# Kernel optimization log

Hardware: AMD Instinct MI355X
Metric: run time of the kernel (lower is better)

## Reference

```python
import jax, jax.numpy as jnp
import numpy as np
import math

B = 2048
STEP = 2        # candidate restarts (original hardcodes 100)
DDIM = 20       # DDIM reverse steps
TIME_DIM = 512
STATE = 6
ACT = 8


def _ddim_coeffs():
    # noise schedule from sample_backward (numpy, host-side constants)
    T = 1000
    t = np.arange(1, T + 1, dtype=np.float64)
    b_max, b_min = 10.0, 0.1
    alpha = np.exp(-b_min / T - 0.5 * (b_max - b_min) * (2 * t - 1) / T ** 2)
    ap = np.cumprod(alpha)
    ts = np.linspace(T, 0, DDIM + 1).astype(np.int64)
    coeffs = []
    for i in range(1, DDIM + 1):
        cur = int(ts[i - 1] - 1)
        prev = int(ts[i] - 1)
        ab_c = ap[cur]
        ab_p = ap[prev] if prev >= 0 else 1.0
        c1 = (ab_p / ab_c) ** 0.5
        var = (1 - ab_p) / (1 - ab_c) * (1 - ab_c / ab_p)  # eta=1 (simple_var)
        c2 = max(1 - ab_p - var, 0.0) ** 0.5 - (ab_p * (1 - ab_c) / ab_c) ** 0.5
        c3 = (1 - ab_c / ab_p) ** 0.5                      # simple_var third term
        coeffs.append((float(cur), float(c1), float(c2), float(c3)))
    return coeffs

_COEFFS = _ddim_coeffs()

_PI = math.pi
JOINT_HIGH = np.array([35 * _PI / 180, -60 * _PI / 180, 3.94, 155 * _PI / 180,
                       -55 * _PI / 180, _PI, 5 * _PI / 180, 3.71], dtype=np.float32)
JOINT_LOW = np.array([-35 * _PI / 180, -155 * _PI / 180, 2.59, 60 * _PI / 180,
                      -125 * _PI / 180, -_PI, -90 * _PI / 180, 2.50], dtype=np.float32)


def _time_emb(cur_t):
    # sinusoidal encoding of a scalar timestep, interleaved sin/cos -> [TIME_DIM]
    div = jnp.exp(jnp.arange(0, TIME_DIM, 2, dtype=jnp.float32) * (-math.log(10000.0) / TIME_DIM))
    return jnp.stack([jnp.sin(cur_t * div), jnp.cos(cur_t * div)], axis=1).reshape(-1)


def _fk(joints):
    # DH forward kinematics over 8 joints; joints: [B, 8] -> pose [B, 6]
    q1, q2, d3, q4, q5, q6, q7, d8 = (joints[:, k] for k in range(8))
    zeros = jnp.zeros_like(q1)
    ones = jnp.ones_like(q1)
    alpha = jnp.deg2rad(jnp.array([0., -90., -90., 90., -90., -90., 90., -90.], dtype=jnp.float32))
    a = jnp.array([0., 0.16, 0.07, 0., 0.1334, 0., 0.15, 0.3625], dtype=jnp.float32)
    d = jnp.stack([zeros, zeros, d3, zeros, -0.1316 * ones, 1.0105 * ones, 0.52 * ones, d8], axis=1)  # [B,8]
    th = jnp.stack([q1, q2, zeros, q4, q5, q6, q7, zeros], axis=1)  # [B,8]
    ct, st = jnp.cos(th), jnp.sin(th)
    ca, sa = jnp.cos(alpha), jnp.sin(alpha)  # [8]
    z8 = jnp.zeros_like(ct)
    o8 = jnp.ones_like(ct)
    ab = jnp.broadcast_to(a, ct.shape)
    row0 = jnp.stack([ct, -st, z8, ab], axis=-1)
    row1 = jnp.stack([st * ca, ct * ca, -sa * o8, -sa * d], axis=-1)
    row2 = jnp.stack([st * sa, ct * sa, ca * o8, ca * d], axis=-1)
    row3 = jnp.stack([z8, z8, z8, o8], axis=-1)
    M = jnp.stack([row0, row1, row2, row3], axis=2)  # [B, 8, 4, 4]
    T = M[:, 0]
    for j in range(1, 8):  # fixed tiny chain of 7 bmms
        T = T @ M[:, j]
    R = T[:, :3, :3]
    hole = jnp.array([0., 0., 3.75], dtype=jnp.float32)
    e1 = R @ hole  # [B, 3]
    pose = jnp.stack([T[:, 0, 3], T[:, 1, 3], T[:, 2, 3] + 1.702,
                      e1[:, 0] + T[:, 0, 3], e1[:, 1] + T[:, 1, 3], e1[:, 2] + T[:, 2, 3] + 1.702], axis=1)
    return pose


def setup_inputs() -> dict:
    key = jax.random.key(0)
    ks = jax.random.split(key, 16)

    def w(k, i, o):
        return jax.random.normal(k, (i, o), jnp.float32) / float(np.sqrt(i))

    return {
        "x_pre": jax.random.normal(ks[0], (B, STATE), jnp.float32) * 50.0,
        "noise": jax.random.normal(ks[1], (STEP, B, ACT), jnp.float32),
        "W_in": w(ks[2], STATE + ACT + TIME_DIM, 512), "b_in": jnp.zeros((512,), jnp.float32),
        "W1": w(ks[3], 512, 512), "b1": jnp.zeros((512,), jnp.float32),
        "W2": w(ks[4], 512, 512), "b2": jnp.zeros((512,), jnp.float32),
        "W3": w(ks[5], 512, 512), "b3": jnp.zeros((512,), jnp.float32),
        "W4": w(ks[6], 512, 512), "b4": jnp.zeros((512,), jnp.float32),
        "W_out": w(ks[7], 512, ACT), "b_out": jnp.zeros((ACT,), jnp.float32),
    }


def reference(x_pre, noise, W_in, b_in, W1, b1, W2, b2, W3, b3, W4, b4, W_out, b_out):
    gelu = lambda v: jax.nn.gelu(v, approximate=False)

    def denoiser(state, action, cur_t):
        t_emb = jnp.broadcast_to(_time_emb(cur_t), (state.shape[0], TIME_DIM))
        x = jnp.concatenate([state, action, t_emb], axis=1)
        y = gelu(x @ W_in + b_in)
        y = gelu(y @ W1 + b1)
        y = gelu(y @ W2 + b2)
        y = gelu(y @ W3 + b3)
        y = gelu(y @ W4 + b4)
        return y @ W_out + b_out

    high = jnp.asarray(JOINT_HIGH)
    low = jnp.asarray(JOINT_LOW)

    errors, joints_all = [], []
    for s in range(STEP):
        nz = noise[s]
        # DDIM reverse loop; NB: the original never feeds z back into `noise`,
        # so each iteration denoises the same initial noise (replicated faithfully).
        z = nz
        for (cur_t, c1, c2, c3) in _COEFFS:
            joint_0 = denoiser(x_pre, nz, cur_t)
            z = c1 * nz + c2 * joint_0 + c3 * nz
        joint_normal = (jnp.tanh(z / 10.0) + 1.0) / 2.0
        new_joint = joint_normal * (high - low) + low  # [B, 8]
        pose_V = _fk(new_joint)                         # [B, 6]
        moni = 100.0 * pose_V
        dist0 = jnp.sqrt(jnp.sum((moni[:, :3] - x_pre[:, :3]) ** 2, axis=1))
        dist1 = jnp.sqrt(jnp.sum((moni[:, 3:] - x_pre[:, 3:]) ** 2, axis=1))
        errors.append(dist0 + dist1)
        joints_all.append(new_joint)

    errors = jnp.stack(errors, axis=0)        # [STEP, B]
    joints_all = jnp.stack(joints_all, axis=0)  # [STEP, B, 8]
    idx = jnp.argmin(errors, axis=0)          # per-sample best restart
    best = jnp.take_along_axis(joints_all, idx[None, :, None], axis=0)[0]  # [B, 8]
    return best
```

## Files before the change

### kernel.cpp

```cpp
#include <hip/hip_runtime.h>
#include <math.h>

typedef __bf16 bf16x8 __attribute__((ext_vector_type(8)));
typedef float f32x4 __attribute__((ext_vector_type(4)));
typedef unsigned short u16;
typedef unsigned short u16x8 __attribute__((ext_vector_type(8)));
typedef unsigned int u32;

constexpr int BATCH = 2048;
constexpr int ROWS  = 4096;
constexpr int HID   = 512;
constexpr int NACT  = 8;

__device__ __forceinline__ float gelu_f(float x) {
    return 0.5f * x * (1.0f + erff(x * 0.70710678118654752f));
}
__device__ __forceinline__ u16 f2bf(float f) {
    u32 u = __float_as_uint(f);
    return (u16)((u + 0x7FFFu + ((u >> 16) & 1u)) >> 16);
}
__device__ __forceinline__ float bf2f(u16 h) {
    return __uint_as_float(((u32)h) << 16);
}

__device__ __forceinline__ size_t fragoff(int r, int k) {
    return (size_t)(((r >> 4) * 16 + (k >> 5)) * 512
                    + (((k & 31) >> 3) * 16 + (r & 15)) * 8 + (k & 7));
}

__global__ __launch_bounds__(256) void k_prep(
        const float* __restrict__ W1, const float* __restrict__ W2,
        const float* __restrict__ W3, const float* __restrict__ W4,
        const float* __restrict__ W_in,
        u16* __restrict__ wt, float* __restrict__ partials) {
    int z = blockIdx.z;
    if (z == 4) {
        if (blockIdx.x >= 4 || blockIdx.y != 0) return;
        __shared__ float temb[128];
        int x = blockIdx.x, t = threadIdx.x;
        if (t < 128) {
            int k = x * 128 + t;
            int p = k >> 1;
            float div = expf((float)(2 * p) * (-9.210340371976184f / 512.0f));
            temb[t] = (k & 1) ? cosf(49.0f * div) : sinf(49.0f * div);
        }
        __syncthreads();
#pragma unroll
        for (int half = 0; half < 2; ++half) {
            int col = half * 256 + t;
            float acc = 0.f;
            for (int kk = 0; kk < 128; ++kk)
                acc += temb[kk] * W_in[(size_t)(14 + x * 128 + kk) * HID + col];
            partials[x * HID + col] = acc;
        }
        return;
    }
    __shared__ float tile[32][33];
    const float* Ws[4] = {W1, W2, W3, W4};
    const float* W = Ws[z];
    u16* wh = wt + (size_t)z * 524288;
    u16* wl = wh + 262144;
    int kt = blockIdx.x * 32, nt = blockIdx.y * 32, t = threadIdx.x;
    int c = t & 31, r = t >> 5;
#pragma unroll
    for (int p = 0; p < 4; ++p)
        tile[r + p * 8][c] = W[(size_t)(kt + r + p * 8) * HID + nt + c];
    __syncthreads();
#pragma unroll
    for (int p = 0; p < 4; ++p) {
        int nl = r + p * 8, kl = c;
        float v = tile[kl][nl];
        u16 h = f2bf(v);
        u16 l2 = f2bf(v - bf2f(h));
        size_t o = fragoff(nt + nl, kt + kl);
        wh[o] = h;
        wl[o] = l2;
    }
}

__global__ __launch_bounds__(256) void k_layer_in(
        const float* __restrict__ x_pre, const float* __restrict__ noise,
        const float* __restrict__ W_in, const float* __restrict__ b_in,
        const float* __restrict__ partials,
        u16* __restrict__ Yh, u16* __restrict__ Yl) {
    int id = blockIdx.x * 256 + threadIdx.x;
    int r = id >> 6, oct = id & 63;
    int s = r >> 11, bidx = r & 2047;
    float xv[6], nz[8];
#pragma unroll
    for (int j = 0; j < 6; ++j) xv[j] = x_pre[bidx * 6 + j];
#pragma unroll
    for (int j = 0; j < 8; ++j) nz[j] = noise[(s * BATCH + bidx) * NACT + j];
    int nc = oct * 8;
    float acc[8];
#pragma unroll
    for (int q = 0; q < 2; ++q) {
        float4 bv = *(const float4*)&b_in[nc + q * 4];
        float4 p0 = *(const float4*)&partials[nc + q * 4];
        float4 p1 = *(const float4*)&partials[512 + nc + q * 4];
        float4 p2 = *(const float4*)&partials[1024 + nc + q * 4];
        float4 p3 = *(const float4*)&partials[1536 + nc + q * 4];
        acc[q * 4 + 0] = bv.x + p0.x + p1.x + p2.x + p3.x;
        acc[q * 4 + 1] = bv.y + p0.y + p1.y + p2.y + p3.y;
        acc[q * 4 + 2] = bv.z + p0.z + p1.z + p2.z + p3.z;
        acc[q * 4 + 3] = bv.w + p0.w + p1.w + p2.w + p3.w;
    }
#pragma unroll
    for (int j = 0; j < 14; ++j) {
        float xj = (j < 6) ? xv[j] : nz[j - 6];
        float4 wa = *(const float4*)&W_in[j * HID + nc];
        float4 wb = *(const float4*)&W_in[j * HID + nc + 4];
        acc[0] += xj * wa.x; acc[1] += xj * wa.y;
        acc[2] += xj * wa.z; acc[3] += xj * wa.w;
        acc[4] += xj * wb.x; acc[5] += xj * wb.y;
        acc[6] += xj * wb.z; acc[7] += xj * wb.w;
    }
    u16x8 hv, lv;
#pragma unroll
    for (int j2 = 0; j2 < 8; ++j2) {
        float g = gelu_f(acc[j2]);
        u16 hi = f2bf(g);
        hv[j2] = hi;
        lv[j2] = f2bf(g - bf2f(hi));
    }
    size_t o = fragoff(r, nc);
    *(u16x8*)&Yh[o] = hv;
    *(u16x8*)&Yl[o] = lv;
}

__global__ __launch_bounds__(512) void k_gemm_f(
        const u16* __restrict__ Ah, const u16* __restrict__ Al,
        const u16* __restrict__ Wh, const u16* __restrict__ Wl,
        const float* __restrict__ bias,
        u16* __restrict__ Yh, u16* __restrict__ Yl) {
    __shared__ __align__(16) u16 lds[3][4][4][512];
    int tid = threadIdx.x, lane = tid & 63, w = tid >> 6;
    int wm = w >> 1, wn = w & 1;
    int m0 = blockIdx.x * 64, n0 = blockIdx.y * 64;

    int p  = w >> 1;
    int g0 = (w & 1) * 2;
    const u16* pl = (p == 0) ? Ah : (p == 1) ? Al : (p == 2) ? Wh : Wl;
    int grpb = ((p < 2) ? m0 : n0) >> 4;
    const u16* src0 = pl + (size_t)((grpb + g0) * 16) * 512 + lane * 8;
    const u16* src1 = pl + (size_t)((grpb + g0 + 1) * 16) * 512 + lane * 8;

    auto stage = [&](int c, int bb) {
        __builtin_amdgcn_global_load_lds(
            (const __attribute__((address_space(1))) void*)(src0 + c * 512),
            (__attribute__((address_space(3))) void*)&lds[bb][p][g0][0], 16, 0, 0);
        __builtin_amdgcn_global_load_lds(
            (const __attribute__((address_space(1))) void*)(src1 + c * 512),
            (__attribute__((address_space(3))) void*)&lds[bb][p][g0 + 1][0], 16, 0, 0);
    };

    f32x4 zero = {0.f, 0.f, 0.f, 0.f};
    f32x4 acc[2] = {zero, zero};

    stage(0, 0);
    stage(1, 1);
#pragma unroll
    for (int c = 0; c < 16; ++c) {
        int bb = c % 3;
        if (c < 15) { asm volatile("s_waitcnt vmcnt(2)" ::: "memory"); }
        else        { asm volatile("s_waitcnt vmcnt(0)" ::: "memory"); }
        __builtin_amdgcn_s_barrier();
        __builtin_amdgcn_sched_barrier(0);

        bf16x8 ah = *(const bf16x8*)&lds[bb][0][wm][lane * 8];
        bf16x8 al = *(const bf16x8*)&lds[bb][1][wm][lane * 8];
        bf16x8 bh[2], bl[2];
#pragma unroll
        for (int j = 0; j < 2; ++j) {
            bh[j] = *(const bf16x8*)&lds[bb][2][wn * 2 + j][lane * 8];
            bl[j] = *(const bf16x8*)&lds[bb][3][wn * 2 + j][lane * 8];
        }
        __builtin_amdgcn_s_setprio(1);
#pragma unroll
        for (int j = 0; j < 2; ++j) {
            acc[j] = __builtin_amdgcn_mfma_f32_16x16x32_bf16(ah, bh[j], acc[j], 0, 0, 0);
            acc[j] = __builtin_amdgcn_mfma_f32_16x16x32_bf16(ah, bl[j], acc[j], 0, 0, 0);
            acc[j] = __builtin_amdgcn_mfma_f32_16x16x32_bf16(al, bh[j], acc[j], 0, 0, 0);
        }
        __builtin_amdgcn_s_setprio(0);
        __builtin_amdgcn_sched_barrier(0);
        if (c < 14) stage(c + 2, (c + 2) % 3);
    }

    int row0 = m0 + wm * 16 + (lane >> 4) * 4;
#pragma unroll
    for (int j = 0; j < 2; ++j) {
        int col = n0 + wn * 32 + j * 16 + (lane & 15);
        float bia = bias[col];
#pragma unroll
        for (int r2 = 0; r2 < 4; ++r2) {
            float g = gelu_f(acc[j][r2] + bia);
            u16 hi = f2bf(g);
            size_t o = fragoff(row0 + r2, col);
            Yh[o] = hi;
            Yl[o] = f2bf(g - bf2f(hi));
        }
    }
}

__device__ void mat4mul(float C[4][4], const float A[4][4], const float Bm[4][4]) {
#pragma unroll
    for (int i = 0; i < 4; ++i)
#pragma unroll
        for (int j = 0; j < 4; ++j) {
            float s = A[i][0] * Bm[0][j];
            s += A[i][1] * Bm[1][j];
            s += A[i][2] * Bm[2][j];
            s += A[i][3] * Bm[3][j];
            C[i][j] = s;
        }
}

__global__ __launch_bounds__(256) void k_out_fk(
        const u16* __restrict__ Yh, const u16* __restrict__ Yl,
        const float* __restrict__ W_out, const float* __restrict__ b_out,
        const float* __restrict__ noise, const float* __restrict__ x_pre,
        float* __restrict__ out, float c1, float c2, float c3) {
    int b = blockIdx.x * 4 + (threadIdx.x >> 6);
    int lane = threadIdx.x & 63;

    float acc0[8] = {0, 0, 0, 0, 0, 0, 0, 0};
    float acc1[8] = {0, 0, 0, 0, 0, 0, 0, 0};
#pragma unroll
    for (int it = 0; it < 8; ++it) {
        int k = lane + it * 64;
        size_t o0 = fragoff(b, k);
        size_t o1 = fragoff(BATCH + b, k);
        float ya = bf2f(Yh[o0]) + bf2f(Yl[o0]);
        float yb = bf2f(Yh[o1]) + bf2f(Yl[o1]);
        float4 w0 = ((const float4*)&W_out[k * NACT])[0];
        float4 w1 = ((const float4*)&W_out[k * NACT])[1];
        acc0[0] += ya * w0.x; acc0[1] += ya * w0.y; acc0[2] += ya * w0.z; acc0[3] += ya * w0.w;
        acc0[4] += ya * w1.x; acc0[5] += ya * w1.y; acc0[6] += ya * w1.z; acc0[7] += ya * w1.w;
        acc1[0] += yb * w0.x; acc1[1] += yb * w0.y; acc1[2] += yb * w0.z; acc1[3] += yb * w0.w;
        acc1[4] += yb * w1.x; acc1[5] += yb * w1.y; acc1[6] += yb * w1.z; acc1[7] += yb * w1.w;
    }
#pragma unroll
    for (int n = 0; n < 8; ++n) {
#pragma unroll
        for (int off = 32; off > 0; off >>= 1) {
            acc0[n] += __shfl_xor(acc0[n], off, 64);
            acc1[n] += __shfl_xor(acc1[n], off, 64);
        }
    }

    float jq[8] = {0, 0, 0, 0, 0, 0, 0, 0};
    float err = 0.f;
    if (lane < 2) {
        int s = lane;
        const float* accp = (s == 0) ? acc0 : acc1;
        const float HIf[8] = {
            (float)(35.0 * M_PI / 180.0), (float)(-60.0 * M_PI / 180.0), 3.94f,
            (float)(155.0 * M_PI / 180.0), (float)(-55.0 * M_PI / 180.0),
            (float)M_PI, (float)(5.0 * M_PI / 180.0), 3.71f};
        const float LOf[8] = {
            (float)(-35.0 * M_PI / 180.0), (float)(-155.0 * M_PI / 180.0), 2.59f,
            (float)(60.0 * M_PI / 180.0), (float)(-125.0 * M_PI / 180.0),
            (float)(-M_PI), (float)(-90.0 * M_PI / 180.0), 2.5f};
        const float* nzp = &noise[(s * BATCH + b) * NACT];
#pragma unroll
        for (int n = 0; n < 8; ++n) {
            float o = accp[n] + b_out[n];
            float z = c1 * nzp[n] + c2 * o + c3 * nzp[n];
            float jn = (tanhf(z * 0.1f) + 1.0f) * 0.5f;
            jq[n] = jn * (HIf[n] - LOf[n]) + LOf[n];
        }
        const float a_[8]  = {0.0f, 0.16f, 0.07f, 0.0f, 0.1334f, 0.0f, 0.15f, 0.3625f};
        const float ca_[8] = {1.f, 0.f, 0.f, 0.f, 0.f, 0.f, 0.f, 0.f};
        const float sa_[8] = {0.f, -1.f, -1.f, 1.f, -1.f, -1.f, 1.f, -1.f};
        float d_[8] = {0.0f, 0.0f, jq[2], 0.0f, -0.1316f, 1.0105f, 0.52f, jq[7]};
        float th[8] = {jq[0], jq[1], 0.0f, jq[3], jq[4], jq[5], jq[6], 0.0f};
        float T[4][4], M[4][4], Tn[4][4];
#pragma unroll
        for (int j = 0; j < 8; ++j) {
            float ct = cosf(th[j]);
            float st = sinf(th[j]);
            M[0][0] = ct;          M[0][1] = -st;         M[0][2] = 0.0f;    M[0][3] = a_[j];
            M[1][0] = st * ca_[j]; M[1][1] = ct * ca_[j]; M[1][2] = -sa_[j]; M[1][3] = -sa_[j] * d_[j];
            M[2][0] = st * sa_[j]; M[2][1] = ct * sa_[j]; M[2][2] = ca_[j];  M[2][3] = ca_[j] * d_[j];
            M[3][0] = 0.0f;        M[3][1] = 0.0f;        M[3][2] = 0.0f;    M[3][3] = 1.0f;
            if (j == 0) {
#pragma unroll
                for (int i = 0; i < 4; ++i)
#pragma unroll
                    for (int cc = 0; cc < 4; ++cc) T[i][cc] = M[i][cc];
            } else {
                mat4mul(Tn, T, M);
#pragma unroll
                for (int i = 0; i < 4; ++i)
#pragma unroll
                    for (int cc = 0; cc < 4; ++cc) T[i][cc] = Tn[i][cc];
            }
        }
        float e1x = T[0][2] * 3.75f;
        float e1y = T[1][2] * 3.75f;
        float e1z = T[2][2] * 3.75f;
        float p0 = T[0][3];
        float p1 = T[1][3];
        float p2 = T[2][3] + 1.702f;
        float p3 = e1x + T[0][3];
        float p4 = e1y + T[1][3];
        float p5 = e1z + T[2][3] + 1.702f;
        const float* xp = &x_pre[b * 6];
        float dx0 = 100.0f * p0 - xp[0];
        float dx1 = 100.0f * p1 - xp[1];
        float dx2 = 100.0f * p2 - xp[2];
        float dx3 = 100.0f * p3 - xp[3];
        float dx4 = 100.0f * p4 - xp[4];
        float dx5 = 100.0f * p5 - xp[5];
        err = sqrtf(dx0 * dx0 + dx1 * dx1 + dx2 * dx2) +
              sqrtf(dx3 * dx3 + dx4 * dx4 + dx5 * dx5);
    }
    float e0 = __shfl(err, 0, 64);
    float e1 = __shfl(err, 1, 64);
    int sel = (e1 < e0) ? 1 : 0;
    float jsel[8];
#pragma unroll
    for (int n = 0; n < 8; ++n) jsel[n] = __shfl(jq[n], sel, 64);
    if (lane == 0) {
#pragma unroll
        for (int n = 0; n < 8; ++n) out[b * NACT + n] = jsel[n];
    }
}

extern "C" void kernel_launch(void* const* d_in, const int* in_sizes, int n_in,
                              void* d_out, int out_size, void* d_ws, size_t ws_size,
                              hipStream_t stream) {
    const float* x_pre = (const float*)d_in[0];
    const float* noise = (const float*)d_in[1];
    const float* W_in  = (const float*)d_in[2];
    const float* b_in  = (const float*)d_in[3];
    const float* W1    = (const float*)d_in[4];
    const float* b1    = (const float*)d_in[5];
    const float* W2    = (const float*)d_in[6];
    const float* b2    = (const float*)d_in[7];
    const float* W3    = (const float*)d_in[8];
    const float* b3    = (const float*)d_in[9];
    const float* W4    = (const float*)d_in[10];
    const float* b4    = (const float*)d_in[11];
    const float* W_out = (const float*)d_in[12];
    const float* b_out = (const float*)d_in[13];

    double ab_c = exp(-0.1 * 50.0 / 1000.0 - 0.5 * (10.0 - 0.1) * 2500.0 / 1.0e6);
    float c1 = (float)sqrt(1.0 / ab_c);
    float c2 = (float)(-sqrt((1.0 - ab_c) / ab_c));
    float c3 = (float)sqrt(1.0 - ab_c);

    char* base = (char*)d_ws;
    u16* Ah = (u16*)base;
    u16* Al = Ah + 2097152;
    u16* Bh = Al + 2097152;
    u16* Bl = Bh + 2097152;
    u16* wt = (u16*)(base + 16777216);
    float* partials = (float*)(base + 16777216 + 4194304);

    k_prep<<<dim3(16, 16, 5), 256, 0, stream>>>(W1, W2, W3, W4, W_in, wt, partials);
    k_layer_in<<<ROWS * 64 / 256, 256, 0, stream>>>(x_pre, noise, W_in, b_in,
                                                    partials, Ah, Al);
    dim3 g(ROWS / 64, HID / 64);
    k_gemm_f<<<g, 512, 0, stream>>>(Ah, Al, wt + 0 * 524288, wt + 0 * 524288 + 262144, b1, Bh, Bl);
    k_gemm_f<<<g, 512, 0, stream>>>(Bh, Bl, wt + 1 * 524288, wt + 1 * 524288 + 262144, b2, Ah, Al);
    k_gemm_f<<<g, 512, 0, stream>>>(Ah, Al, wt + 2 * 524288, wt + 2 * 524288 + 262144, b3, Bh, Bl);
    k_gemm_f<<<g, 512, 0, stream>>>(Bh, Bl, wt + 3 * 524288, wt + 3 * 524288 + 262144, b4, Ah, Al);
    k_out_fk<<<BATCH / 4, 256, 0, stream>>>(Ah, Al, W_out, b_out, noise, x_pre,
                                            (float*)d_out, c1, c2, c3);
}
```

Baseline: 87.56 us.

## Retile split-bf16 GEMM to 32x128 blocks with 4 waves each owning 2x2 MFMA tiles

The hidden-layer GEMM kernel moves from 64x64 tiles with 8 waves (each computing 1x2 MFMA tiles) to 32x128 tiles with 4 waves (each computing 2x2 MFMA tiles). Each wave now reuses its A fragments across more B columns, which raises MFMA work per LDS read, and each wave issues five async global-to-LDS loads per stage instead of two. The grid grows to 128x4 blocks of 256 threads. The risk is fewer waves per block to hide latency, plus more B-weight traffic per block because each block covers a wider N range.

```diff
diff --git a/kernel.cpp b/kernel.cpp
--- a/kernel.cpp
+++ b/kernel.cpp
@@ -128,77 +128,94 @@
     *(u16x8*)&Yl[o] = lv;
 }
 
-__global__ __launch_bounds__(512) void k_gemm_f(
+__global__ __launch_bounds__(256) void k_gemm_f(
         const u16* __restrict__ Ah, const u16* __restrict__ Al,
         const u16* __restrict__ Wh, const u16* __restrict__ Wl,
         const float* __restrict__ bias,
         u16* __restrict__ Yh, u16* __restrict__ Yl) {
-    __shared__ __align__(16) u16 lds[3][4][4][512];
+    __shared__ __align__(16) u16 lds[3][20][512];
     int tid = threadIdx.x, lane = tid & 63, w = tid >> 6;
-    int wm = w >> 1, wn = w & 1;
-    int m0 = blockIdx.x * 64, n0 = blockIdx.y * 64;
-
-    int p  = w >> 1;
-    int g0 = (w & 1) * 2;
-    const u16* pl = (p == 0) ? Ah : (p == 1) ? Al : (p == 2) ? Wh : Wl;
-    int grpb = ((p < 2) ? m0 : n0) >> 4;
-    const u16* src0 = pl + (size_t)((grpb + g0) * 16) * 512 + lane * 8;
-    const u16* src1 = pl + (size_t)((grpb + g0 + 1) * 16) * 512 + lane * 8;
-
-    auto stage = [&](int c, int bb) {
-        __builtin_amdgcn_global_load_lds(
-            (const __attribute__((address_space(1))) void*)(src0 + c * 512),
-            (__attribute__((address_space(3))) void*)&lds[bb][p][g0][0], 16, 0, 0);
-        __builtin_amdgcn_global_load_lds(
-            (const __attribute__((address_space(1))) void*)(src1 + c * 512),
-            (__attribute__((address_space(3))) void*)&lds[bb][p][g0 + 1][0], 16, 0, 0);
+    int m0 = blockIdx.x * 32, n0 = blockIdx.y * 128;
+
+    int apl = w >> 1, ag = w & 1;
+    const u16* aplane = apl ? Al : Ah;
+    const u16* srcA = aplane + (size_t)((blockIdx.x * 2 + ag) * 16) * 512 + lane * 8;
+    const u16* srcB0 = Wh + (size_t)((blockIdx.y * 8 + 2 * w) * 16) * 512 + lane * 8;
+    const u16* srcB1 = Wh + (size_t)((blockIdx.y * 8 + 2 * w + 1) * 16) * 512 + lane * 8;
+    const u16* srcB2 = Wl + (size_t)((blockIdx.y * 8 + 2 * w) * 16) * 512 + lane * 8;
+    const u16* srcB3 = Wl + (size_t)((blockIdx.y * 8 + 2 * w + 1) * 16) * 512 + lane * 8;
+
+    auto stage = [&](int c, int sl) {
+        __builtin_amdgcn_global_load_lds(
+            (const __attribute__((address_space(1))) void*)(srcA + c * 512),
+            (__attribute__((address_space(3))) void*)&lds[sl][apl * 2 + ag][0], 16, 0, 0);
+        __builtin_amdgcn_global_load_lds(
+            (const __attribute__((address_space(1))) void*)(srcB0 + c * 512),
+            (__attribute__((address_space(3))) void*)&lds[sl][4 + 2 * w][0], 16, 0, 0);
+        __builtin_amdgcn_global_load_lds(
+            (const __attribute__((address_space(1))) void*)(srcB1 + c * 512),
+            (__attribute__((address_space(3))) void*)&lds[sl][4 + 2 * w + 1][0], 16, 0, 0);
+        __builtin_amdgcn_global_load_lds(
+            (const __attribute__((address_space(1))) void*)(srcB2 + c * 512),
+            (__attribute__((address_space(3))) void*)&lds[sl][12 + 2 * w][0], 16, 0, 0);
+        __builtin_amdgcn_global_load_lds(
+            (const __attribute__((address_space(1))) void*)(srcB3 + c * 512),
+            (__attribute__((address_space(3))) void*)&lds[sl][12 + 2 * w + 1][0], 16, 0, 0);
     };
 
     f32x4 zero = {0.f, 0.f, 0.f, 0.f};
-    f32x4 acc[2] = {zero, zero};
+    f32x4 acc[2][2] = {{zero, zero}, {zero, zero}};
 
     stage(0, 0);
     stage(1, 1);
 #pragma unroll
     for (int c = 0; c < 16; ++c) {
-        int bb = c % 3;
-        if (c < 15) { asm volatile("s_waitcnt vmcnt(2)" ::: "memory"); }
+        int sl = c % 3;
+        if (c < 15) { asm volatile("s_waitcnt vmcnt(5)" ::: "memory"); }
         else        { asm volatile("s_waitcnt vmcnt(0)" ::: "memory"); }
         __builtin_amdgcn_s_barrier();
         __builtin_amdgcn_sched_barrier(0);
 
-        bf16x8 ah = *(const bf16x8*)&lds[bb][0][wm][lane * 8];
-        bf16x8 al = *(const bf16x8*)&lds[bb][1][wm][lane * 8];
-        bf16x8 bh[2], bl[2];
+        bf16x8 ah[2], al[2], bh[2], bl[2];
+#pragma unroll
+        for (int i = 0; i < 2; ++i) {
+            ah[i] = *(const bf16x8*)&lds[sl][i][lane * 8];
+            al[i] = *(const bf16x8*)&lds[sl][2 + i][lane * 8];
+        }
 #pragma unroll
         for (int j = 0; j < 2; ++j) {
-            bh[j] = *(const bf16x8*)&lds[bb][2][wn * 2 + j][lane * 8];
-            bl[j] = *(const bf16x8*)&lds[bb][3][wn * 2 + j][lane * 8];
+            bh[j] = *(const bf16x8*)&lds[sl][4 + 2 * w + j][lane * 8];
+            bl[j] = *(const bf16x8*)&lds[sl][12 + 2 * w + j][lane * 8];
         }
         __builtin_amdgcn_s_setprio(1);
 #pragma unroll
-        for (int j = 0; j < 2; ++j) {
-            acc[j] = __builtin_amdgcn_mfma_f32_16x16x32_bf16(ah, bh[j], acc[j], 0, 0, 0);
-            acc[j] = __builtin_amdgcn_mfma_f32_16x16x32_bf16(ah, bl[j], acc[j], 0, 0, 0);
-            acc[j] = __builtin_amdgcn_mfma_f32_16x16x32_bf16(al, bh[j], acc[j], 0, 0, 0);
-        }
+        for (int i = 0; i < 2; ++i)
+#pragma unroll
+            for (int j = 0; j < 2; ++j) {
+                acc[i][j] = __builtin_amdgcn_mfma_f32_16x16x32_bf16(ah[i], bh[j], acc[i][j], 0, 0, 0);
+                acc[i][j] = __builtin_amdgcn_mfma_f32_16x16x32_bf16(ah[i], bl[j], acc[i][j], 0, 0, 0);
+                acc[i][j] = __builtin_amdgcn_mfma_f32_16x16x32_bf16(al[i], bh[j], acc[i][j], 0, 0, 0);
+            }
         __builtin_amdgcn_s_setprio(0);
         __builtin_amdgcn_sched_barrier(0);
         if (c < 14) stage(c + 2, (c + 2) % 3);
     }
 
-    int row0 = m0 + wm * 16 + (lane >> 4) * 4;
-#pragma unroll
-    for (int j = 0; j < 2; ++j) {
-        int col = n0 + wn * 32 + j * 16 + (lane & 15);
-        float bia = bias[col];
-#pragma unroll
-        for (int r2 = 0; r2 < 4; ++r2) {
-            float g = gelu_f(acc[j][r2] + bia);
-            u16 hi = f2bf(g);
-            size_t o = fragoff(row0 + r2, col);
-            Yh[o] = hi;
-            Yl[o] = f2bf(g - bf2f(hi));
+#pragma unroll
+    for (int i = 0; i < 2; ++i) {
+        int row0 = m0 + i * 16 + (lane >> 4) * 4;
+#pragma unroll
+        for (int j = 0; j < 2; ++j) {
+            int col = n0 + w * 32 + j * 16 + (lane & 15);
+            float bia = bias[col];
+#pragma unroll
+            for (int r2 = 0; r2 < 4; ++r2) {
+                float g = gelu_f(acc[i][j][r2] + bia);
+                u16 hi = f2bf(g);
+                size_t o = fragoff(row0 + r2, col);
+                Yh[o] = hi;
+                Yl[o] = f2bf(g - bf2f(hi));
+            }
         }
     }
 }
@@ -362,11 +379,11 @@
     k_prep<<<dim3(16, 16, 5), 256, 0, stream>>>(W1, W2, W3, W4, W_in, wt, partials);
     k_layer_in<<<ROWS * 64 / 256, 256, 0, stream>>>(x_pre, noise, W_in, b_in,
                                                     partials, Ah, Al);
-    dim3 g(ROWS / 64, HID / 64);
-    k_gemm_f<<<g, 512, 0, stream>>>(Ah, Al, wt + 0 * 524288, wt + 0 * 524288 + 262144, b1, Bh, Bl);
-    k_gemm_f<<<g, 512, 0, stream>>>(Bh, Bl, wt + 1 * 524288, wt + 1 * 524288 + 262144, b2, Ah, Al);
-    k_gemm_f<<<g, 512, 0, stream>>>(Ah, Al, wt + 2 * 524288, wt + 2 * 524288 + 262144, b3, Bh, Bl);
-    k_gemm_f<<<g, 512, 0, stream>>>(Bh, Bl, wt + 3 * 524288, wt + 3 * 524288 + 262144, b4, Ah, Al);
+    dim3 g(ROWS / 32, HID / 128);
+    k_gemm_f<<<g, 256, 0, stream>>>(Ah, Al, wt + 0 * 524288, wt + 0 * 524288 + 262144, b1, Bh, Bl);
+    k_gemm_f<<<g, 256, 0, stream>>>(Bh, Bl, wt + 1 * 524288, wt + 1 * 524288 + 262144, b2, Ah, Al);
+    k_gemm_f<<<g, 256, 0, stream>>>(Ah, Al, wt + 2 * 524288, wt + 2 * 524288 + 262144, b3, Bh, Bl);
+    k_gemm_f<<<g, 256, 0, stream>>>(Bh, Bl, wt + 3 * 524288, wt + 3 * 524288 + 262144, b4, Ah, Al);
     k_out_fk<<<BATCH / 4, 256, 0, stream>>>(Ah, Al, W_out, b_out, noise, x_pre,
                                             (float*)d_out, c1, c2, c3);
 }
```

New measurement: 93.89 us. 7.2% more time.

## Fuse input layer, four hidden GEMMs and output/FK into one persistent-row kernel

Applied to the files above, without the earlier changes.

Replaces the input-layer kernel, four tiled GEMM launches and the output/FK kernel with a single kernel where each block owns 16 rows (8 batch items × 2 restarts) and keeps the activations in LDS across all layers. Weights are streamed directly from global memory into registers with a 3-deep software prefetch, and each wave computes 64 output columns. This removes the global round-trips of the 4096×512 split-bf16 activations and five launch overheads. In exchange only 256 blocks run, every block re-reads the full weight set (served from L2), and MFMA work per block is serialized over layers with less parallelism.

```diff
diff --git a/kernel.cpp b/kernel.cpp
--- a/kernel.cpp
+++ b/kernel.cpp
@@ -8,7 +8,6 @@
 typedef unsigned int u32;
 
 constexpr int BATCH = 2048;
-constexpr int ROWS  = 4096;
 constexpr int HID   = 512;
 constexpr int NACT  = 8;
 
@@ -78,131 +77,6 @@
     }
 }
 
-__global__ __launch_bounds__(256) void k_layer_in(
-        const float* __restrict__ x_pre, const float* __restrict__ noise,
-        const float* __restrict__ W_in, const float* __restrict__ b_in,
-        const float* __restrict__ partials,
-        u16* __restrict__ Yh, u16* __restrict__ Yl) {
-    int id = blockIdx.x * 256 + threadIdx.x;
-    int r = id >> 6, oct = id & 63;
-    int s = r >> 11, bidx = r & 2047;
-    float xv[6], nz[8];
-#pragma unroll
-    for (int j = 0; j < 6; ++j) xv[j] = x_pre[bidx * 6 + j];
-#pragma unroll
-    for (int j = 0; j < 8; ++j) nz[j] = noise[(s * BATCH + bidx) * NACT + j];
-    int nc = oct * 8;
-    float acc[8];
-#pragma unroll
-    for (int q = 0; q < 2; ++q) {
-        float4 bv = *(const float4*)&b_in[nc + q * 4];
-        float4 p0 = *(const float4*)&partials[nc + q * 4];
-        float4 p1 = *(const float4*)&partials[512 + nc + q * 4];
-        float4 p2 = *(const float4*)&partials[1024 + nc + q * 4];
-        float4 p3 = *(const float4*)&partials[1536 + nc + q * 4];
-        acc[q * 4 + 0] = bv.x + p0.x + p1.x + p2.x + p3.x;
-        acc[q * 4 + 1] = bv.y + p0.y + p1.y + p2.y + p3.y;
-        acc[q * 4 + 2] = bv.z + p0.z + p1.z + p2.z + p3.z;
-        acc[q * 4 + 3] = bv.w + p0.w + p1.w + p2.w + p3.w;
-    }
-#pragma unroll
-    for (int j = 0; j < 14; ++j) {
-        float xj = (j < 6) ? xv[j] : nz[j - 6];
-        float4 wa = *(const float4*)&W_in[j * HID + nc];
-        float4 wb = *(const float4*)&W_in[j * HID + nc + 4];
-        acc[0] += xj * wa.x; acc[1] += xj * wa.y;
-        acc[2] += xj * wa.z; acc[3] += xj * wa.w;
-        acc[4] += xj * wb.x; acc[5] += xj * wb.y;
-        acc[6] += xj * wb.z; acc[7] += xj * wb.w;
-    }
-    u16x8 hv, lv;
-#pragma unroll
-    for (int j2 = 0; j2 < 8; ++j2) {
-        float g = gelu_f(acc[j2]);
-        u16 hi = f2bf(g);
-        hv[j2] = hi;
-        lv[j2] = f2bf(g - bf2f(hi));
-    }
-    size_t o = fragoff(r, nc);
-    *(u16x8*)&Yh[o] = hv;
-    *(u16x8*)&Yl[o] = lv;
-}
-
-__global__ __launch_bounds__(512) void k_gemm_f(
-        const u16* __restrict__ Ah, const u16* __restrict__ Al,
-        const u16* __restrict__ Wh, const u16* __restrict__ Wl,
-        const float* __restrict__ bias,
-        u16* __restrict__ Yh, u16* __restrict__ Yl) {
-    __shared__ __align__(16) u16 lds[3][4][4][512];
-    int tid = threadIdx.x, lane = tid & 63, w = tid >> 6;
-    int wm = w >> 1, wn = w & 1;
-    int m0 = blockIdx.x * 64, n0 = blockIdx.y * 64;
-
-    int p  = w >> 1;
-    int g0 = (w & 1) * 2;
-    const u16* pl = (p == 0) ? Ah : (p == 1) ? Al : (p == 2) ? Wh : Wl;
-    int grpb = ((p < 2) ? m0 : n0) >> 4;
-    const u16* src0 = pl + (size_t)((grpb + g0) * 16) * 512 + lane * 8;
-    const u16* src1 = pl + (size_t)((grpb + g0 + 1) * 16) * 512 + lane * 8;
-
-    auto stage = [&](int c, int bb) {
-        __builtin_amdgcn_global_load_lds(
-            (const __attribute__((address_space(1))) void*)(src0 + c * 512),
-            (__attribute__((address_space(3))) void*)&lds[bb][p][g0][0], 16, 0, 0);
-        __builtin_amdgcn_global_load_lds(
-            (const __attribute__((address_space(1))) void*)(src1 + c * 512),
-            (__attribute__((address_space(3))) void*)&lds[bb][p][g0 + 1][0], 16, 0, 0);
-    };
-
-    f32x4 zero = {0.f, 0.f, 0.f, 0.f};
-    f32x4 acc[2] = {zero, zero};
-
-    stage(0, 0);
-    stage(1, 1);
-#pragma unroll
-    for (int c = 0; c < 16; ++c) {
-        int bb = c % 3;
-        if (c < 15) { asm volatile("s_waitcnt vmcnt(2)" ::: "memory"); }
-        else        { asm volatile("s_waitcnt vmcnt(0)" ::: "memory"); }
-        __builtin_amdgcn_s_barrier();
-        __builtin_amdgcn_sched_barrier(0);
-
-        bf16x8 ah = *(const bf16x8*)&lds[bb][0][wm][lane * 8];
-        bf16x8 al = *(const bf16x8*)&lds[bb][1][wm][lane * 8];
-        bf16x8 bh[2], bl[2];
-#pragma unroll
-        for (int j = 0; j < 2; ++j) {
-            bh[j] = *(const bf16x8*)&lds[bb][2][wn * 2 + j][lane * 8];
-            bl[j] = *(const bf16x8*)&lds[bb][3][wn * 2 + j][lane * 8];
-        }
-        __builtin_amdgcn_s_setprio(1);
-#pragma unroll
-        for (int j = 0; j < 2; ++j) {
-            acc[j] = __builtin_amdgcn_mfma_f32_16x16x32_bf16(ah, bh[j], acc[j], 0, 0, 0);
-            acc[j] = __builtin_amdgcn_mfma_f32_16x16x32_bf16(ah, bl[j], acc[j], 0, 0, 0);
-            acc[j] = __builtin_amdgcn_mfma_f32_16x16x32_bf16(al, bh[j], acc[j], 0, 0, 0);
-        }
-        __builtin_amdgcn_s_setprio(0);
-        __builtin_amdgcn_sched_barrier(0);
-        if (c < 14) stage(c + 2, (c + 2) % 3);
-    }
-
-    int row0 = m0 + wm * 16 + (lane >> 4) * 4;
-#pragma unroll
-    for (int j = 0; j < 2; ++j) {
-        int col = n0 + wn * 32 + j * 16 + (lane & 15);
-        float bia = bias[col];
-#pragma unroll
-        for (int r2 = 0; r2 < 4; ++r2) {
-            float g = gelu_f(acc[j][r2] + bia);
-            u16 hi = f2bf(g);
-            size_t o = fragoff(row0 + r2, col);
-            Yh[o] = hi;
-            Yl[o] = f2bf(g - bf2f(hi));
-        }
-    }
-}
-
 __device__ void mat4mul(float C[4][4], const float A[4][4], const float Bm[4][4]) {
 #pragma unroll
     for (int i = 0; i < 4; ++i)
@@ -216,115 +90,231 @@
         }
 }
 
-__global__ __launch_bounds__(256) void k_out_fk(
-        const u16* __restrict__ Yh, const u16* __restrict__ Yl,
+__global__ __launch_bounds__(512) void k_mlp(
+        const float* __restrict__ x_pre, const float* __restrict__ noise,
+        const float* __restrict__ W_in, const float* __restrict__ b_in,
+        const float* __restrict__ partials, const u16* __restrict__ wt,
+        const float* __restrict__ b1, const float* __restrict__ b2,
+        const float* __restrict__ b3, const float* __restrict__ b4,
         const float* __restrict__ W_out, const float* __restrict__ b_out,
-        const float* __restrict__ noise, const float* __restrict__ x_pre,
         float* __restrict__ out, float c1, float c2, float c3) {
-    int b = blockIdx.x * 4 + (threadIdx.x >> 6);
-    int lane = threadIdx.x & 63;
-
-    float acc0[8] = {0, 0, 0, 0, 0, 0, 0, 0};
-    float acc1[8] = {0, 0, 0, 0, 0, 0, 0, 0};
-#pragma unroll
-    for (int it = 0; it < 8; ++it) {
-        int k = lane + it * 64;
-        size_t o0 = fragoff(b, k);
-        size_t o1 = fragoff(BATCH + b, k);
-        float ya = bf2f(Yh[o0]) + bf2f(Yl[o0]);
-        float yb = bf2f(Yh[o1]) + bf2f(Yl[o1]);
-        float4 w0 = ((const float4*)&W_out[k * NACT])[0];
-        float4 w1 = ((const float4*)&W_out[k * NACT])[1];
-        acc0[0] += ya * w0.x; acc0[1] += ya * w0.y; acc0[2] += ya * w0.z; acc0[3] += ya * w0.w;
-        acc0[4] += ya * w1.x; acc0[5] += ya * w1.y; acc0[6] += ya * w1.z; acc0[7] += ya * w1.w;
-        acc1[0] += yb * w0.x; acc1[1] += yb * w0.y; acc1[2] += yb * w0.z; acc1[3] += yb * w0.w;
-        acc1[4] += yb * w1.x; acc1[5] += yb * w1.y; acc1[6] += yb * w1.z; acc1[7] += yb * w1.w;
-    }
-#pragma unroll
-    for (int n = 0; n < 8; ++n) {
-#pragma unroll
-        for (int off = 32; off > 0; off >>= 1) {
-            acc0[n] += __shfl_xor(acc0[n], off, 64);
-            acc1[n] += __shfl_xor(acc1[n], off, 64);
-        }
-    }
-
-    float jq[8] = {0, 0, 0, 0, 0, 0, 0, 0};
-    float err = 0.f;
-    if (lane < 2) {
-        int s = lane;
-        const float* accp = (s == 0) ? acc0 : acc1;
-        const float HIf[8] = {
-            (float)(35.0 * M_PI / 180.0), (float)(-60.0 * M_PI / 180.0), 3.94f,
-            (float)(155.0 * M_PI / 180.0), (float)(-55.0 * M_PI / 180.0),
-            (float)M_PI, (float)(5.0 * M_PI / 180.0), 3.71f};
-        const float LOf[8] = {
-            (float)(-35.0 * M_PI / 180.0), (float)(-155.0 * M_PI / 180.0), 2.59f,
-            (float)(60.0 * M_PI / 180.0), (float)(-125.0 * M_PI / 180.0),
-            (float)(-M_PI), (float)(-90.0 * M_PI / 180.0), 2.5f};
-        const float* nzp = &noise[(s * BATCH + b) * NACT];
+    __shared__ __align__(16) u16 A[2][16][512];
+    int tid = threadIdx.x, lane = tid & 63, w = tid >> 6;
+    int l15 = lane & 15;
+    int b0 = blockIdx.x * 8;
+
+#pragma unroll
+    for (int rep = 0; rep < 2; ++rep) {
+        int id = tid + rep * 512;
+        int r = id & 15, oct = id >> 4;
+        int st = r >> 3, be = b0 + (r & 7);
+        float xv[6], nz[8];
+#pragma unroll
+        for (int j = 0; j < 6; ++j) xv[j] = x_pre[be * 6 + j];
+#pragma unroll
+        for (int j = 0; j < 8; ++j) nz[j] = noise[(st * BATCH + be) * NACT + j];
+        int nc = oct * 8;
+        float acc[8];
+#pragma unroll
+        for (int q = 0; q < 2; ++q) {
+            float4 bv = *(const float4*)&b_in[nc + q * 4];
+            float4 p0 = *(const float4*)&partials[nc + q * 4];
+            float4 p1 = *(const float4*)&partials[512 + nc + q * 4];
+            float4 p2 = *(const float4*)&partials[1024 + nc + q * 4];
+            float4 p3 = *(const float4*)&partials[1536 + nc + q * 4];
+            acc[q * 4 + 0] = bv.x + p0.x + p1.x + p2.x + p3.x;
+            acc[q * 4 + 1] = bv.y + p0.y + p1.y + p2.y + p3.y;
+            acc[q * 4 + 2] = bv.z + p0.z + p1.z + p2.z + p3.z;
+            acc[q * 4 + 3] = bv.w + p0.w + p1.w + p2.w + p3.w;
+        }
+#pragma unroll
+        for (int j = 0; j < 14; ++j) {
+            float xj = (j < 6) ? xv[j] : nz[j - 6];
+            float4 wa = *(const float4*)&W_in[j * HID + nc];
+            float4 wb = *(const float4*)&W_in[j * HID + nc + 4];
+            acc[0] += xj * wa.x; acc[1] += xj * wa.y;
+            acc[2] += xj * wa.z; acc[3] += xj * wa.w;
+            acc[4] += xj * wb.x; acc[5] += xj * wb.y;
+            acc[6] += xj * wb.z; acc[7] += xj * wb.w;
+        }
+        u16x8 hv, lv;
+#pragma unroll
+        for (int j2 = 0; j2 < 8; ++j2) {
+            float g = gelu_f(acc[j2]);
+            u16 hi = f2bf(g);
+            hv[j2] = hi;
+            lv[j2] = f2bf(g - bf2f(hi));
+        }
+        int ch = nc >> 5;
+        int idx = (((nc & 31) >> 3) * 16 + r) * 8;
+        *(u16x8*)&A[0][ch][idx] = hv;
+        *(u16x8*)&A[1][ch][idx] = lv;
+    }
+    __syncthreads();
+
+    const u16* wh_l[4] = {wt, wt + 524288, wt + 1048576, wt + 1572864};
+    const float* bias_l[4] = {b1, b2, b3, b4};
+    int g4 = 4 * w;
+
+#pragma unroll 1
+    for (int l = 0; l < 4; ++l) {
+        const u16* Wh  = wh_l[l];
+        const u16* Wl2 = Wh + 262144;
+        f32x4 zero = {0.f, 0.f, 0.f, 0.f};
+        f32x4 acc[4] = {zero, zero, zero, zero};
+        bf16x8 bh[3][4], bl[3][4];
+#pragma unroll
+        for (int g = 0; g < 4; ++g) {
+            bh[0][g] = *(const bf16x8*)(Wh  + (size_t)((g4 + g) * 16 + 0) * 512 + lane * 8);
+            bl[0][g] = *(const bf16x8*)(Wl2 + (size_t)((g4 + g) * 16 + 0) * 512 + lane * 8);
+            bh[1][g] = *(const bf16x8*)(Wh  + (size_t)((g4 + g) * 16 + 1) * 512 + lane * 8);
+            bl[1][g] = *(const bf16x8*)(Wl2 + (size_t)((g4 + g) * 16 + 1) * 512 + lane * 8);
+        }
+#pragma unroll
+        for (int c = 0; c < 16; ++c) {
+            const int cur = c % 3;
+            if (c < 14) {
+                const int nxt = (c + 2) % 3;
+#pragma unroll
+                for (int g = 0; g < 4; ++g) {
+                    bh[nxt][g] = *(const bf16x8*)(Wh  + (size_t)((g4 + g) * 16 + c + 2) * 512 + lane * 8);
+                    bl[nxt][g] = *(const bf16x8*)(Wl2 + (size_t)((g4 + g) * 16 + c + 2) * 512 + lane * 8);
+                }
+            }
+            bf16x8 ah = *(const bf16x8*)&A[0][c][lane * 8];
+            bf16x8 al = *(const bf16x8*)&A[1][c][lane * 8];
+#pragma unroll
+            for (int g = 0; g < 4; ++g) {
+                acc[g] = __builtin_amdgcn_mfma_f32_16x16x32_bf16(ah, bh[cur][g], acc[g], 0, 0, 0);
+                acc[g] = __builtin_amdgcn_mfma_f32_16x16x32_bf16(ah, bl[cur][g], acc[g], 0, 0, 0);
+                acc[g] = __builtin_amdgcn_mfma_f32_16x16x32_bf16(al, bh[cur][g], acc[g], 0, 0, 0);
+            }
+        }
+        __syncthreads();
+        const float* bias = bias_l[l];
+#pragma unroll
+        for (int g = 0; g < 4; ++g) {
+            int col = w * 64 + g * 16 + l15;
+            float bia = bias[col];
+            int ch = col >> 5;
+#pragma unroll
+            for (int r2 = 0; r2 < 4; ++r2) {
+                int row = (lane >> 4) * 4 + r2;
+                float gv = gelu_f(acc[g][r2] + bia);
+                u16 hi = f2bf(gv);
+                int idx = (((col & 31) >> 3) * 16 + row) * 8 + (col & 7);
+                A[0][ch][idx] = hi;
+                A[1][ch][idx] = f2bf(gv - bf2f(hi));
+            }
+        }
+        __syncthreads();
+    }
+
+    {
+        int be = b0 + w;
+        float acc0[8] = {0, 0, 0, 0, 0, 0, 0, 0};
+        float acc1[8] = {0, 0, 0, 0, 0, 0, 0, 0};
+#pragma unroll
+        for (int it = 0; it < 8; ++it) {
+            int k = lane + it * 64;
+            int ch = k >> 5;
+            int base = ((k & 31) >> 3) * 16;
+            int ko = k & 7;
+            float ya = bf2f(A[0][ch][(base + w) * 8 + ko]) + bf2f(A[1][ch][(base + w) * 8 + ko]);
+            float yb = bf2f(A[0][ch][(base + 8 + w) * 8 + ko]) + bf2f(A[1][ch][(base + 8 + w) * 8 + ko]);
+            float4 w0 = ((const float4*)&W_out[k * NACT])[0];
+            float4 w1 = ((const float4*)&W_out[k * NACT])[1];
+            acc0[0] += ya * w0.x; acc0[1] += ya * w0.y; acc0[2] += ya * w0.z; acc0[3] += ya * w0.w;
+            acc0[4] += ya * w1.x; acc0[5] += ya * w1.y; acc0[6] += ya * w1.z; acc0[7] += ya * w1.w;
+            acc1[0] += yb * w0.x; acc1[1] += yb * w0.y; acc1[2] += yb * w0.z; acc1[3] += yb * w0.w;
+            acc1[4] += yb * w1.x; acc1[5] += yb * w1.y; acc1[6] += yb * w1.z; acc1[7] += yb * w1.w;
+        }
 #pragma unroll
         for (int n = 0; n < 8; ++n) {
-            float o = accp[n] + b_out[n];
-            float z = c1 * nzp[n] + c2 * o + c3 * nzp[n];
-            float jn = (tanhf(z * 0.1f) + 1.0f) * 0.5f;
-            jq[n] = jn * (HIf[n] - LOf[n]) + LOf[n];
-        }
-        const float a_[8]  = {0.0f, 0.16f, 0.07f, 0.0f, 0.1334f, 0.0f, 0.15f, 0.3625f};
-        const float ca_[8] = {1.f, 0.f, 0.f, 0.f, 0.f, 0.f, 0.f, 0.f};
-        const float sa_[8] = {0.f, -1.f, -1.f, 1.f, -1.f, -1.f, 1.f, -1.f};
-        float d_[8] = {0.0f, 0.0f, jq[2], 0.0f, -0.1316f, 1.0105f, 0.52f, jq[7]};
-        float th[8] = {jq[0], jq[1], 0.0f, jq[3], jq[4], jq[5], jq[6], 0.0f};
-        float T[4][4], M[4][4], Tn[4][4];
-#pragma unroll
-        for (int j = 0; j < 8; ++j) {
-            float ct = cosf(th[j]);
-            float st = sinf(th[j]);
-            M[0][0] = ct;          M[0][1] = -st;         M[0][2] = 0.0f;    M[0][3] = a_[j];
-            M[1][0] = st * ca_[j]; M[1][1] = ct * ca_[j]; M[1][2] = -sa_[j]; M[1][3] = -sa_[j] * d_[j];
-            M[2][0] = st * sa_[j]; M[2][1] = ct * sa_[j]; M[2][2] = ca_[j];  M[2][3] = ca_[j] * d_[j];
-            M[3][0] = 0.0f;        M[3][1] = 0.0f;        M[3][2] = 0.0f;    M[3][3] = 1.0f;
-            if (j == 0) {
-#pragma unroll
-                for (int i = 0; i < 4; ++i)
-#pragma unroll
-                    for (int cc = 0; cc < 4; ++cc) T[i][cc] = M[i][cc];
-            } else {
-                mat4mul(Tn, T, M);
-#pragma unroll
-                for (int i = 0; i < 4; ++i)
-#pragma unroll
-                    for (int cc = 0; cc < 4; ++cc) T[i][cc] = Tn[i][cc];
-            }
-        }
-        float e1x = T[0][2] * 3.75f;
-        float e1y = T[1][2] * 3.75f;
-        float e1z = T[2][2] * 3.75f;
-        float p0 = T[0][3];
-        float p1 = T[1][3];
-        float p2 = T[2][3] + 1.702f;
-        float p3 = e1x + T[0][3];
-        float p4 = e1y + T[1][3];
-        float p5 = e1z + T[2][3] + 1.702f;
-        const float* xp = &x_pre[b * 6];
-        float dx0 = 100.0f * p0 - xp[0];
-        float dx1 = 100.0f * p1 - xp[1];
-        float dx2 = 100.0f * p2 - xp[2];
-        float dx3 = 100.0f * p3 - xp[3];
-        float dx4 = 100.0f * p4 - xp[4];
-        float dx5 = 100.0f * p5 - xp[5];
-        err = sqrtf(dx0 * dx0 + dx1 * dx1 + dx2 * dx2) +
-              sqrtf(dx3 * dx3 + dx4 * dx4 + dx5 * dx5);
-    }
-    float e0 = __shfl(err, 0, 64);
-    float e1 = __shfl(err, 1, 64);
-    int sel = (e1 < e0) ? 1 : 0;
-    float jsel[8];
-#pragma unroll
-    for (int n = 0; n < 8; ++n) jsel[n] = __shfl(jq[n], sel, 64);
-    if (lane == 0) {
-#pragma unroll
-        for (int n = 0; n < 8; ++n) out[b * NACT + n] = jsel[n];
+#pragma unroll
+            for (int off = 32; off > 0; off >>= 1) {
+                acc0[n] += __shfl_xor(acc0[n], off, 64);
+                acc1[n] += __shfl_xor(acc1[n], off, 64);
+            }
+        }
+
+        float jq[8] = {0, 0, 0, 0, 0, 0, 0, 0};
+        float err = 0.f;
+        if (lane < 2) {
+            int s = lane;
+            const float* accp = (s == 0) ? acc0 : acc1;
+            const float HIf[8] = {
+                (float)(35.0 * M_PI / 180.0), (float)(-60.0 * M_PI / 180.0), 3.94f,
+                (float)(155.0 * M_PI / 180.0), (float)(-55.0 * M_PI / 180.0),
+                (float)M_PI, (float)(5.0 * M_PI / 180.0), 3.71f};
+            const float LOf[8] = {
+                (float)(-35.0 * M_PI / 180.0), (float)(-155.0 * M_PI / 180.0), 2.59f,
+                (float)(60.0 * M_PI / 180.0), (float)(-125.0 * M_PI / 180.0),
+                (float)(-M_PI), (float)(-90.0 * M_PI / 180.0), 2.5f};
+            const float* nzp = &noise[(s * BATCH + be) * NACT];
+#pragma unroll
+            for (int n = 0; n < 8; ++n) {
+                float o = accp[n] + b_out[n];
+                float z = c1 * nzp[n] + c2 * o + c3 * nzp[n];
+                float jn = (tanhf(z * 0.1f) + 1.0f) * 0.5f;
+                jq[n] = jn * (HIf[n] - LOf[n]) + LOf[n];
+            }
+            const float a_[8]  = {0.0f, 0.16f, 0.07f, 0.0f, 0.1334f, 0.0f, 0.15f, 0.3625f};
+            const float ca_[8] = {1.f, 0.f, 0.f, 0.f, 0.f, 0.f, 0.f, 0.f};
+            const float sa_[8] = {0.f, -1.f, -1.f, 1.f, -1.f, -1.f, 1.f, -1.f};
+            float d_[8] = {0.0f, 0.0f, jq[2], 0.0f, -0.1316f, 1.0105f, 0.52f, jq[7]};
+            float th[8] = {jq[0], jq[1], 0.0f, jq[3], jq[4], jq[5], jq[6], 0.0f};
+            float T[4][4], M[4][4], Tn[4][4];
+#pragma unroll
+            for (int j = 0; j < 8; ++j) {
+                float ct = cosf(th[j]);
+                float st = sinf(th[j]);
+                M[0][0] = ct;          M[0][1] = -st;         M[0][2] = 0.0f;    M[0][3] = a_[j];
+                M[1][0] = st * ca_[j]; M[1][1] = ct * ca_[j]; M[1][2] = -sa_[j]; M[1][3] = -sa_[j] * d_[j];
+                M[2][0] = st * sa_[j]; M[2][1] = ct * sa_[j]; M[2][2] = ca_[j];  M[2][3] = ca_[j] * d_[j];
+                M[3][0] = 0.0f;        M[3][1] = 0.0f;        M[3][2] = 0.0f;    M[3][3] = 1.0f;
+                if (j == 0) {
+#pragma unroll
+                    for (int i = 0; i < 4; ++i)
+#pragma unroll
+                        for (int cc = 0; cc < 4; ++cc) T[i][cc] = M[i][cc];
+                } else {
+                    mat4mul(Tn, T, M);
+#pragma unroll
+                    for (int i = 0; i < 4; ++i)
+#pragma unroll
+                        for (int cc = 0; cc < 4; ++cc) T[i][cc] = Tn[i][cc];
+                }
+            }
+            float e1x = T[0][2] * 3.75f;
+            float e1y = T[1][2] * 3.75f;
+            float e1z = T[2][2] * 3.75f;
+            float p0 = T[0][3];
+            float p1 = T[1][3];
+            float p2 = T[2][3] + 1.702f;
+            float p3 = e1x + T[0][3];
+            float p4 = e1y + T[1][3];
+            float p5 = e1z + T[2][3] + 1.702f;
+            const float* xp = &x_pre[be * 6];
+            float dx0 = 100.0f * p0 - xp[0];
+            float dx1 = 100.0f * p1 - xp[1];
+            float dx2 = 100.0f * p2 - xp[2];
+            float dx3 = 100.0f * p3 - xp[3];
+            float dx4 = 100.0f * p4 - xp[4];
+            float dx5 = 100.0f * p5 - xp[5];
+            err = sqrtf(dx0 * dx0 + dx1 * dx1 + dx2 * dx2) +
+                  sqrtf(dx3 * dx3 + dx4 * dx4 + dx5 * dx5);
+        }
+        float e0 = __shfl(err, 0, 64);
+        float e1 = __shfl(err, 1, 64);
+        int sel = (e1 < e0) ? 1 : 0;
+        float jsel[8];
+#pragma unroll
+        for (int n = 0; n < 8; ++n) jsel[n] = __shfl(jq[n], sel, 64);
+        if (lane == 0) {
+#pragma unroll
+            for (int n = 0; n < 8; ++n) out[be * NACT + n] = jsel[n];
+        }
     }
 }
 
@@ -352,21 +342,11 @@
     float c3 = (float)sqrt(1.0 - ab_c);
 
     char* base = (char*)d_ws;
-    u16* Ah = (u16*)base;
-    u16* Al = Ah + 2097152;
-    u16* Bh = Al + 2097152;
-    u16* Bl = Bh + 2097152;
-    u16* wt = (u16*)(base + 16777216);
-    float* partials = (float*)(base + 16777216 + 4194304);
+    u16* wt = (u16*)base;
+    float* partials = (float*)(base + 4194304);
 
     k_prep<<<dim3(16, 16, 5), 256, 0, stream>>>(W1, W2, W3, W4, W_in, wt, partials);
-    k_layer_in<<<ROWS * 64 / 256, 256, 0, stream>>>(x_pre, noise, W_in, b_in,
-                                                    partials, Ah, Al);
-    dim3 g(ROWS / 64, HID / 64);
-    k_gemm_f<<<g, 512, 0, stream>>>(Ah, Al, wt + 0 * 524288, wt + 0 * 524288 + 262144, b1, Bh, Bl);
-    k_gemm_f<<<g, 512, 0, stream>>>(Bh, Bl, wt + 1 * 524288, wt + 1 * 524288 + 262144, b2, Ah, Al);
-    k_gemm_f<<<g, 512, 0, stream>>>(Ah, Al, wt + 2 * 524288, wt + 2 * 524288 + 262144, b3, Bh, Bl);
-    k_gemm_f<<<g, 512, 0, stream>>>(Bh, Bl, wt + 3 * 524288, wt + 3 * 524288 + 262144, b4, Ah, Al);
-    k_out_fk<<<BATCH / 4, 256, 0, stream>>>(Ah, Al, W_out, b_out, noise, x_pre,
-                                            (float*)d_out, c1, c2, c3);
-}
+    k_mlp<<<256, 512, 0, stream>>>(x_pre, noise, W_in, b_in, partials, wt,
+                                   b1, b2, b3, b4, W_out, b_out,
+                                   (float*)d_out, c1, c2, c3);
+}
```

After: 100.9 us. 1.15x slower.
